# Performance work log

Measured on AMD Instinct MI355X. Metric: run time of the kernel, lower is better.

The kernel has to match this reference:

```python
import jax, jax.numpy as jnp
import numpy as np

SEQ_LEN, BATCH, INPUT, HID, LAYERS, TARGET_LEN = 120, 2048, 6, 64, 4, 120


def _cell(x_t, h, c, Wih, Whh, b):
    # torch LSTM gate order: input, forget, cell(g), output
    gates = x_t @ Wih.T + h @ Whh.T + b  # [B, 4H]
    i, f, g, o = jnp.split(gates, 4, axis=-1)
    c_new = jax.nn.sigmoid(f) * c + jax.nn.sigmoid(i) * jnp.tanh(g)
    h_new = jax.nn.sigmoid(o) * jnp.tanh(c_new)
    return h_new, c_new


def _stack_step(h, c, x_t, Wih0, Wih, Whh, b):
    # one time step through all stacked layers; h, c: [L, B, H]
    hs, cs = [], []
    inp = x_t
    L = Whh.shape[0]
    for l in range(L):
        W = Wih0 if l == 0 else Wih[l - 1]
        hn, cn = _cell(inp, h[l], c[l], W, Whh[l], b[l])
        hs.append(hn)
        cs.append(cn)
        inp = hn
    return jnp.stack(hs), jnp.stack(cs), inp


def setup_inputs() -> dict:
    key = jax.random.key(0)
    ks = jax.random.split(key, 11)
    s = 1.0 / np.sqrt(HID)  # torch LSTM uniform init scale
    u = lambda k, shp: jax.random.uniform(k, shp, jnp.float32, -s, s)
    return {
        "x": jax.random.normal(ks[0], (SEQ_LEN, BATCH, INPUT), jnp.float32),
        "enc_Wih0": u(ks[1], (4 * HID, INPUT)),
        "enc_Wih": u(ks[2], (LAYERS - 1, 4 * HID, HID)),
        "enc_Whh": u(ks[3], (LAYERS, 4 * HID, HID)),
        "enc_b": u(ks[4], (LAYERS, 4 * HID)),
        "dec_Wih0": u(ks[5], (4 * HID, INPUT)),
        "dec_Wih": u(ks[6], (LAYERS - 1, 4 * HID, HID)),
        "dec_Whh": u(ks[7], (LAYERS, 4 * HID, HID)),
        "dec_b": u(ks[8], (LAYERS, 4 * HID)),
        "lin_W": u(ks[9], (INPUT, HID)),
        "lin_b": u(ks[10], (INPUT,)),
        "target_len": TARGET_LEN,
    }


def reference(x, enc_Wih0, enc_Wih, enc_Whh, enc_b,
              dec_Wih0, dec_Wih, dec_Whh, dec_b, lin_W, lin_b, target_len):
    L, B, H = enc_Whh.shape[0], x.shape[1], enc_Whh.shape[-1]
    h0 = jnp.zeros((L, B, H), x.dtype)

    # ---- encoder: stacked LSTM over the input sequence (zero init state) ----
    def enc_step(carry, x_t):
        h, c = carry
        h, c, _ = _stack_step(h, c, x_t, enc_Wih0, enc_Wih, enc_Whh, enc_b)
        return (h, c), None

    (h, c), _ = jax.lax.scan(enc_step, (h0, h0), x)

    # ---- decoder: recursive one-step decode for target_len steps ----
    def dec_step(carry, _):
        h, c, inp = carry
        h, c, top = _stack_step(h, c, inp, dec_Wih0, dec_Wih, dec_Whh, dec_b)
        out = top @ lin_W.T + lin_b  # [B, INPUT]
        return (h, c, out), out

    last_in = x[-1]  # decoder seeded with last observed frame
    _, outputs = jax.lax.scan(dec_step, (h, c, last_in), None, length=target_len)
    return outputs  # [target_len, B, INPUT]
```

## Files before the change

### kernel.cpp

```cpp
#include <hip/hip_runtime.h>


#define S_LEN 120
#define BATCH 2048
#define NIN   6
#define H     64
#define NL    4
#define TLEN  120

#define HPAD 72

#define FRAGS_HALF 60
#define PACK_H8    (2 * FRAGS_HALF * 4 * 64)
#define PROJ_H8    (2 * 64)
#define NPACK      ((PACK_H8 + PROJ_H8) * 8)
#define EPACK_EL   (256 * 64 * 8)
#define NTOT       (NPACK + EPACK_EL)

#define WS_HOFF (768 * 1024)
#define WS_COFF (WS_HOFF + 1024 * 1024)

#define PERM(kk) ((((kk) & 3) << 4) | ((kk) >> 2))
#define PI(c)    ((((c) & 15) << 2) | ((c) >> 4))

typedef _Float16 h8    __attribute__((ext_vector_type(8)));
typedef _Float16 hh2   __attribute__((ext_vector_type(2)));
typedef float    f32x4 __attribute__((ext_vector_type(4)));

__device__ __forceinline__ void bar_lgkm() {
  asm volatile("s_waitcnt lgkmcnt(0)\n\ts_barrier" ::: "memory");
}

__global__ void prep_weights(const float* __restrict__ eWih0,
                             const float* __restrict__ eWih,
                             const float* __restrict__ eWhh,
                             const float* __restrict__ dWih0,
                             const float* __restrict__ dWih,
                             const float* __restrict__ dWhh,
                             const float* __restrict__ linW,
                             _Float16* __restrict__ wq) {
  int idx = blockIdx.x * blockDim.x + threadIdx.x;
  if (idx >= NTOT) return;

  if (idx >= NPACK) {
    int p    = idx - NPACK;
    int j    = p & 7;
    int lane = (p >> 3) & 63;
    int fe   = p >> 9;
    int kt   = fe & 3, nt = (fe >> 2) & 15, l = fe >> 6;
    int g    = nt * 16 + (lane & 15);
    int koff = ((lane >> 4) << 3) + j;
    float v = 0.0f;
    if (l == 0) {
      if (kt == 0)      v = (koff < NIN) ? eWih0[g * NIN + koff] : 0.0f;
      else if (kt == 1) v = 0.0f;
      else { int kk = (kt - 2) * 32 + koff; v = eWhh[g * H + PERM(kk)]; }
    } else {
      if (kt < 2) { int kk = kt * 32 + koff;
                    v = eWih[((l - 1) * 256 + g) * H + PERM(kk)]; }
      else        { int kk = (kt - 2) * 32 + koff;
                    v = eWhh[(l * 256 + g) * H + PERM(kk)]; }
    }
    wq[idx] = (_Float16)v;
    return;
  }

  if (idx >= PACK_H8 * 8) {
    int p    = idx - PACK_H8 * 8;
    int j    = p & 7;
    int lane = (p >> 3) & 63;
    int fr   = p >> 9;
    int m    = lane & 15;
    int k    = fr * 32 + ((lane >> 4) << 3) + j;
    wq[idx] = (_Float16)((m < NIN) ? linW[m * H + k] : 0.0f);
    return;
  }

  const int j    = idx & 7;
  const int lane = (idx >> 3) & 63;
  const int wv   = (idx >> 9) & 3;
  const int fh   = idx >> 11;
  const int f    = fh % FRAGS_HALF;
  const int half = fh / FRAGS_HALF;
  const float* Wi0 = half ? dWih0 : eWih0;
  const float* Wi  = half ? dWih  : eWih;
  const float* Wh  = half ? dWhh  : eWhh;
  int l, q, kt;
  if (f < 12) { l = 0; q = f / 3; kt = f % 3; }
  else        { int ff = f - 12; l = 1 + ff / 16; ff %= 16; q = ff / 4; kt = ff % 4; }
  const int g    = q * 64 + wv * 16 + (lane & 15);
  const int k_in = ((lane >> 4) << 3) + j;
  float v;
  if (l == 0) {
    if (kt == 0) v = (k_in < NIN) ? Wi0[g * NIN + k_in] : 0.0f;
    else         v = Wh[g * H + (kt - 1) * 32 + k_in];
  } else {
    if (kt < 2) v = Wi[((l - 1) * 256 + g) * H + kt * 32 + k_in];
    else        v = Wh[(l * 256 + g) * H + (kt - 2) * 32 + k_in];
  }
  wq[idx] = (_Float16)v;
}

__device__ __forceinline__ float rcpf(float x) { return __builtin_amdgcn_rcpf(x); }
__device__ __forceinline__ f32x4 mf(h8 a, h8 b, f32x4 c) {
  return __builtin_amdgcn_mfma_f32_16x16x32_f16(a, b, c, 0, 0, 0);
}
#define SPLAT(v) ((f32x4){(v), (v), (v), (v)})

__device__ __forceinline__ float ew_one(float gi, float gf, float gg, float go,
                                        float& c) {
  gg = fminf(fmaxf(gg, -20.0f), 20.0f);
  float eni = __expf(-gi);
  float e2g = __expf(2.0f * gg);
  float enf = __expf(-gf);
  float eno = __expf(-go);
  c = c * rcpf(1.0f + enf) + (e2g - 1.0f) * rcpf((1.0f + eni) * (e2g + 1.0f));
  float cc = fminf(fmaxf(c, -20.0f), 20.0f);
  float e2c = __expf(2.0f * cc);
  return (e2c - 1.0f) * rcpf((1.0f + eno) * (e2c + 1.0f));
}

__device__ __forceinline__ void cell_ew(f32x4 g0, f32x4 g1, f32x4 g2, f32x4 g3,
                                        f32x4& c, _Float16* outbuf,
                                        int quad, int r16, int lw) {
  #pragma unroll
  for (int r = 0; r < 4; r++) {
    float cv = c[r];
    float hv = ew_one(g0[r], g1[r], g2[r], g3[r], cv);
    c[r] = cv;
    outbuf[(quad * 4 + r) * HPAD + lw * 16 + r16] = (_Float16)hv;
  }
}
__device__ __forceinline__ void fireH(const h8 (&w)[16], h8 ai0, h8 ai1,
                                      const f32x4 (&ac)[4], f32x4& c,
                                      _Float16* outbuf, int quad, int r16, int lw) {
  f32x4 g0 = mf(ai1, w[1],  mf(ai0, w[0],  ac[0]));
  f32x4 g1 = mf(ai1, w[5],  mf(ai0, w[4],  ac[1]));
  f32x4 g2 = mf(ai1, w[9],  mf(ai0, w[8],  ac[2]));
  f32x4 g3 = mf(ai1, w[13], mf(ai0, w[12], ac[3]));
  cell_ew(g0, g1, g2, g3, c, outbuf, quad, r16, lw);
}
__device__ __forceinline__ void precH(const h8 (&w)[16], h8 ar0, h8 ar1,
                                      f32x4 b, f32x4 (&ac)[4]) {
  ac[0] = mf(ar1, w[3],  mf(ar0, w[2],  SPLAT(b[0])));
  ac[1] = mf(ar1, w[7],  mf(ar0, w[6],  SPLAT(b[1])));
  ac[2] = mf(ar1, w[11], mf(ar0, w[10], SPLAT(b[2])));
  ac[3] = mf(ar1, w[15], mf(ar0, w[14], SPLAT(b[3])));
}
__device__ __forceinline__ void fire0(const h8 (&w)[12], h8 ax,
                                      const f32x4 (&ac)[4], f32x4& c,
                                      _Float16* outbuf, int quad, int r16, int lw) {
  f32x4 g0 = mf(ax, w[0], ac[0]);
  f32x4 g1 = mf(ax, w[3], ac[1]);
  f32x4 g2 = mf(ax, w[6], ac[2]);
  f32x4 g3 = mf(ax, w[9], ac[3]);
  cell_ew(g0, g1, g2, g3, c, outbuf, quad, r16, lw);
}
__device__ __forceinline__ void prec0(const h8 (&w)[12], h8 ar0, h8 ar1,
                                      f32x4 b, f32x4 (&ac)[4]) {
  ac[0] = mf(ar1, w[2],  mf(ar0, w[1],  SPLAT(b[0])));
  ac[1] = mf(ar1, w[5],  mf(ar0, w[4],  SPLAT(b[1])));
  ac[2] = mf(ar1, w[8],  mf(ar0, w[7],  SPLAT(b[2])));
  ac[3] = mf(ar1, w[11], mf(ar0, w[10], SPLAT(b[3])));
}
__device__ __forceinline__ void readA(const _Float16* buf, int r16, int quad,
                                      h8& a0, h8& a1) {
  a0 = *(const h8*)(buf + r16 * HPAD + quad * 8);
  a1 = *(const h8*)(buf + r16 * HPAD + 32 + quad * 8);
}

__global__ void __launch_bounds__(512, 2)
lstm_enc(const float* __restrict__ X,
         const float* __restrict__ encb,
         const h8* __restrict__ WQ,
         _Float16* __restrict__ hG,
         float* __restrict__ cG) {
  __shared__ _Float16 Hb[NL][2][16][HPAD];
  __shared__ _Float16 Xb[2][16][HPAD];

  const int tid  = threadIdx.x;
  const int wv   = tid >> 6;
  const int lane = tid & 63;
  const int quad = lane >> 4;
  const int r16  = lane & 15;
  const int grp  = wv >> 2;
  const int lw   = wv & 3;
  const int bbase = blockIdx.x * 16;

  {
    float* p = (float*)&Hb[0][0][0][0];
    for (int i = tid; i < 4608; i += 512) p[i] = 0.0f;
    float* px = (float*)&Xb[0][0][0];
    for (int i = tid; i < 1152; i += 512) if (i < 1152) px[i] = 0.0f;
  }
  if (tid < 16 * NIN) {
    int m = tid / NIN, ii = tid - m * NIN;
    Xb[0][m][ii] = (_Float16)X[((size_t)0 * BATCH + bbase + m) * NIN + ii];
  }

  h8 we[8][4];
  #pragma unroll
  for (int q = 0; q < 4; q++)
    #pragma unroll
    for (int cc = 0; cc < 2; cc++)
      #pragma unroll
      for (int kt = 0; kt < 4; kt++)
        we[q * 2 + cc][kt] =
            WQ[(PACK_H8 + PROJ_H8) +
               ((lw * 64 + (q * 4 + 2 * grp + cc) * 4 + kt) * 64 + lane)];
  float ben[8];
  #pragma unroll
  for (int q = 0; q < 4; q++)
    #pragma unroll
    for (int cc = 0; cc < 2; cc++)
      ben[q * 2 + cc] = encb[lw * 256 + q * 64 + (2 * grp + cc) * 16 + r16];

  f32x4 ce[2];
  ce[0] = SPLAT(0.f); ce[1] = SPLAT(0.f);

  const bool pfLane = (wv == 0) && (lane < 48);
  const int  pe0 = lane * 2, pe1 = pe0 + 1;
  const int  pm0 = pe0 / NIN, pc0 = pe0 % NIN;
  const int  pm1 = pe1 / NIN, pc1 = pe1 % NIN;
  float pf0 = 0.f, pf1 = 0.f;
  if (pfLane) {
    const float* xs = X + ((size_t)1 * BATCH + bbase) * NIN;
    pf0 = xs[pe0]; pf1 = xs[pe1];
  }

  __syncthreads();

  #pragma unroll 1
  for (int i = 0; i < S_LEN + NL - 1; i++) {
    const int p = i & 1;
    const bool active = (i >= lw) && (i - lw < S_LEN);
    if (active) {
      const _Float16* inb = (lw == 0) ? &Xb[p][0][0] : &Hb[lw - 1][p ^ 1][0][0];
      const _Float16* rcb = &Hb[lw][p ^ 1][0][0];
      h8 ai0 = *(const h8*)(inb + r16 * HPAD + quad * 8);
      h8 ai1 = {};
      if (lw) ai1 = *(const h8*)(inb + r16 * HPAD + 32 + quad * 8);
      h8 ar0 = *(const h8*)(rcb + r16 * HPAD + quad * 8);
      h8 ar1 = *(const h8*)(rcb + r16 * HPAD + 32 + quad * 8);

      float nf0 = 0.f, nf1 = 0.f;
      if (pfLane && (i + 2 < S_LEN)) {
        const float* xs = X + ((size_t)(i + 2) * BATCH + bbase) * NIN;
        nf0 = xs[pe0]; nf1 = xs[pe1];
      }

      f32x4 a[8];
      #pragma unroll
      for (int j = 0; j < 8; j++) {
        f32x4 t = SPLAT(ben[j]);
        t = mf(ai0, we[j][0], t);
        if (lw) t = mf(ai1, we[j][1], t);
        t = mf(ar0, we[j][2], t);
        t = mf(ar1, we[j][3], t);
        a[j] = t;
      }

      _Float16* wb = &Hb[lw][p][0][0];
      #pragma unroll
      for (int r = 0; r < 4; r++) {
        hh2 hv;
        #pragma unroll
        for (int cc = 0; cc < 2; cc++) {
          float cv = ce[cc][r];
          hv[cc] = (_Float16)ew_one(a[cc][r], a[2 + cc][r],
                                    a[4 + cc][r], a[6 + cc][r], cv);
          ce[cc][r] = cv;
        }
        *(hh2*)(wb + (quad * 4 + r) * HPAD + 4 * r16 + 2 * grp) = hv;
      }

      if (pfLane && (i + 1 < S_LEN)) {
        Xb[p ^ 1][pm0][pc0] = (_Float16)pf0;
        Xb[p ^ 1][pm1][pc1] = (_Float16)pf1;
      }
      pf0 = nf0; pf1 = nf1;
    }
    bar_lgkm();
  }

  #pragma unroll
  for (int cc = 0; cc < 2; cc++)
    #pragma unroll
    for (int r = 0; r < 4; r++)
      cG[((size_t)lw * BATCH + bbase + quad * 4 + r) * H +
         (2 * grp + cc) * 16 + r16] = ce[cc][r];

  #pragma unroll
  for (int u = 0; u < 8; u++) {
    int i2 = tid + u * 512;
    int c = i2 & 63, m = (i2 >> 6) & 15, l = (i2 >> 10) & 3;
    hG[((size_t)l * BATCH + bbase + m) * H + c] =
        Hb[l][(l + 1) & 1][m][PI(c)];
  }
}

__global__ void __launch_bounds__(256, 1)
lstm_dec(const float* __restrict__ X,
         const float* __restrict__ decb,
         const float* __restrict__ linb,
         const h8* __restrict__ WQ,
         const _Float16* __restrict__ hG,
         const float* __restrict__ cG,
         float* __restrict__ out) {
  __shared__ _Float16 Hb[NL][2][16][HPAD];

  const int tid   = threadIdx.x;
  const int lw    = tid >> 6;
  const int lane  = tid & 63;
  const int quad  = lane >> 4;
  const int r16   = lane & 15;
  const int bbase = blockIdx.x * 16;

  #pragma unroll
  for (int u = 0; u < 16; u++) {
    int i2 = tid + u * 256;
    int l = i2 >> 10, m = (i2 >> 6) & 15, c = i2 & 63;
    Hb[l][1][m][c] = hG[((size_t)l * BATCH + bbase + m) * H + c];
  }

  f32x4 cs0, cs1, cs2, cs3;
  #pragma unroll
  for (int r = 0; r < 4; r++) {
    cs0[r] = cG[((size_t)0 * BATCH + bbase + quad * 4 + r) * H + lw * 16 + r16];
    cs1[r] = cG[((size_t)1 * BATCH + bbase + quad * 4 + r) * H + lw * 16 + r16];
    cs2[r] = cG[((size_t)2 * BATCH + bbase + quad * 4 + r) * H + lw * 16 + r16];
    cs3[r] = cG[((size_t)3 * BATCH + bbase + quad * 4 + r) * H + lw * 16 + r16];
  }

  h8 w0[12], w1[16], w2[16], w3[16];
  #pragma unroll
  for (int f = 0; f < 12; f++) w0[f] = WQ[((FRAGS_HALF + f)      * 4 + lw) * 64 + lane];
  #pragma unroll
  for (int f = 0; f < 16; f++) w1[f] = WQ[((FRAGS_HALF + 12 + f) * 4 + lw) * 64 + lane];
  #pragma unroll
  for (int f = 0; f < 16; f++) w2[f] = WQ[((FRAGS_HALF + 28 + f) * 4 + lw) * 64 + lane];
  #pragma unroll
  for (int f = 0; f < 16; f++) w3[f] = WQ[((FRAGS_HALF + 44 + f) * 4 + lw) * 64 + lane];

  f32x4 b0, b1, b2, b3;
  #pragma unroll
  for (int q = 0; q < 4; q++) {
    b0[q] = decb[0 * 256 + q * 64 + lw * 16 + r16];
    b1[q] = decb[1 * 256 + q * 64 + lw * 16 + r16];
    b2[q] = decb[2 * 256 + q * 64 + lw * 16 + r16];
    b3[q] = decb[3 * 256 + q * 64 + lw * 16 + r16];
  }

  h8 lwA0 = WQ[PACK_H8 + lane];
  h8 lwA1 = WQ[PACK_H8 + 64 + lane];
  f32x4 lbq;
  #pragma unroll
  for (int r = 0; r < 4; r++)
    lbq[r] = (quad * 4 + r < NIN) ? linb[quad * 4 + r] : 0.0f;

  h8 xseed = {};
  if (quad == 0) {
    const float* xs = X + ((size_t)(S_LEN - 1) * BATCH + bbase + r16) * NIN;
    #pragma unroll
    for (int j = 0; j < 6; j++) xseed[j] = (_Float16)xs[j];
  }

  __syncthreads();

  f32x4 ac0[4], ac1[4], ac2[4], ac3[4];
  {
    h8 s0, s1;
    readA(&Hb[0][1][0][0], r16, quad, s0, s1); prec0(w0, s0, s1, b0, ac0);
    readA(&Hb[1][1][0][0], r16, quad, s0, s1); precH(w1, s0, s1, b1, ac1);
    readA(&Hb[2][1][0][0], r16, quad, s0, s1); precH(w2, s0, s1, b2, ac2);
  }

  #pragma unroll 1
  for (int t = 0; t < TLEN; t++) {
    const int cur = t & 1, prv = cur ^ 1;
    {
      h8 ar0, ar1;
      readA(&Hb[3][prv][0][0], r16, quad, ar0, ar1);
      h8 ax;
      if (t == 0) {
        ax = xseed;
      } else {
        f32x4 ap = lbq;
        ap = mf(lwA0, ar0, ap);
        ap = mf(lwA1, ar1, ap);
        if (lw == 0) {
          #pragma unroll
          for (int r = 0; r < 4; r++) {
            const int fm = quad * 4 + r;
            if (fm < NIN)
              out[((size_t)(t - 1) * BATCH + bbase + r16) * NIN + fm] = ap[r];
          }
        }
        float x0 = __shfl(ap[0], r16);
        float x1 = __shfl(ap[1], r16);
        float x2 = __shfl(ap[2], r16);
        float x3 = __shfl(ap[3], r16);
        float x4 = __shfl(ap[0], 16 + r16);
        float x5 = __shfl(ap[1], 16 + r16);
        h8 xa = {};
        xa[0] = (_Float16)x0; xa[1] = (_Float16)x1; xa[2] = (_Float16)x2;
        xa[3] = (_Float16)x3; xa[4] = (_Float16)x4; xa[5] = (_Float16)x5;
        h8 zz = {};
        ax = (quad == 0) ? xa : zz;
      }
      precH(w3, ar0, ar1, b3, ac3);
      fire0(w0, ax, ac0, cs0, &Hb[0][cur][0][0], quad, r16, lw);
      bar_lgkm();
    }
    {
      h8 ai0, ai1;
      readA(&Hb[0][cur][0][0], r16, quad, ai0, ai1);
      fireH(w1, ai0, ai1, ac1, cs1, &Hb[1][cur][0][0], quad, r16, lw);
      prec0(w0, ai0, ai1, b0, ac0);
      bar_lgkm();
    }
    {
      h8 ai0, ai1;
      readA(&Hb[1][cur][0][0], r16, quad, ai0, ai1);
      fireH(w2, ai0, ai1, ac2, cs2, &Hb[2][cur][0][0], quad, r16, lw);
      precH(w1, ai0, ai1, b1, ac1);
      bar_lgkm();
    }
    {
      h8 ai0, ai1;
      readA(&Hb[2][cur][0][0], r16, quad, ai0, ai1);
      fireH(w3, ai0, ai1, ac3, cs3, &Hb[3][cur][0][0], quad, r16, lw);
      precH(w2, ai0, ai1, b2, ac2);
      bar_lgkm();
    }
  }

  if (lw == 0) {
    h8 ar0, ar1;
    readA(&Hb[3][1][0][0], r16, quad, ar0, ar1);
    f32x4 ap = lbq;
    ap = mf(lwA0, ar0, ap);
    ap = mf(lwA1, ar1, ap);
    #pragma unroll
    for (int r = 0; r < 4; r++) {
      const int fm = quad * 4 + r;
      if (fm < NIN)
        out[((size_t)(TLEN - 1) * BATCH + bbase + r16) * NIN + fm] = ap[r];
    }
  }
}

extern "C" void kernel_launch(void* const* d_in, const int* in_sizes, int n_in,
                              void* d_out, int out_size, void* d_ws, size_t ws_size,
                              hipStream_t stream) {
  const float* X     = (const float*)d_in[0];
  const float* eWih0 = (const float*)d_in[1];
  const float* eWih  = (const float*)d_in[2];
  const float* eWhh  = (const float*)d_in[3];
  const float* eb    = (const float*)d_in[4];
  const float* dWih0 = (const float*)d_in[5];
  const float* dWih  = (const float*)d_in[6];
  const float* dWhh  = (const float*)d_in[7];
  const float* db    = (const float*)d_in[8];
  const float* lW    = (const float*)d_in[9];
  const float* lb    = (const float*)d_in[10];

  _Float16* wq = (_Float16*)d_ws;
  _Float16* hG = (_Float16*)((char*)d_ws + WS_HOFF);
  float*    cG = (float*)((char*)d_ws + WS_COFF);

  prep_weights<<<(NTOT + 255) / 256, 256, 0, stream>>>(
      eWih0, eWih, eWhh, dWih0, dWih, dWhh, lW, wq);

  lstm_enc<<<BATCH / 16, 512, 0, stream>>>(
      X, eb, (const h8*)wq, hG, cG);

  lstm_dec<<<BATCH / 16, 256, 0, stream>>>(
      X, db, lb, (const h8*)wq, hG, cG, (float*)d_out);
}
```

Baseline: 566.0 us.

## Shrink per-block batch tile to raise block count in encoder and decoder

The encoder now handles 8 batch rows per block instead of 16, and the decoder 4 rows instead of 16. Block counts rise to 256 and 512, so more CUs are busy on this latency-bound recurrence. In the encoder, lanes split the MFMA output rows with a cross-half shuffle so each lane runs fewer elementwise gate updates. The decoder still runs full 16-row MFMA tiles filled with replicated rows, so it repeats work to gain parallelism, and the extra shuffles add per-step latency.

```diff
diff --git a/kernel.cpp b/kernel.cpp
--- a/kernel.cpp
+++ b/kernel.cpp
@@ -185,15 +185,17 @@
   const int r16  = lane & 15;
   const int grp  = wv >> 2;
   const int lw   = wv & 3;
-  const int bbase = blockIdx.x * 16;
+  const bool hi  = quad >= 2;
+  const int rowA = hi ? (quad - 2) * 4 + 2 : quad * 4;
+  const int bbase = blockIdx.x * 8;
 
   {
     float* p = (float*)&Hb[0][0][0][0];
     for (int i = tid; i < 4608; i += 512) p[i] = 0.0f;
     float* px = (float*)&Xb[0][0][0];
-    for (int i = tid; i < 1152; i += 512) if (i < 1152) px[i] = 0.0f;
-  }
-  if (tid < 16 * NIN) {
+    for (int i = tid; i < 1152; i += 512) px[i] = 0.0f;
+  }
+  if (tid < 8 * NIN) {
     int m = tid / NIN, ii = tid - m * NIN;
     Xb[0][m][ii] = (_Float16)X[((size_t)0 * BATCH + bbase + m) * NIN + ii];
   }
@@ -215,18 +217,14 @@
     for (int cc = 0; cc < 2; cc++)
       ben[q * 2 + cc] = encb[lw * 256 + q * 64 + (2 * grp + cc) * 16 + r16];
 
-  f32x4 ce[2];
-  ce[0] = SPLAT(0.f); ce[1] = SPLAT(0.f);
+  float2 ce2[2];
+  ce2[0] = make_float2(0.f, 0.f);
+  ce2[1] = make_float2(0.f, 0.f);
 
   const bool pfLane = (wv == 0) && (lane < 48);
-  const int  pe0 = lane * 2, pe1 = pe0 + 1;
-  const int  pm0 = pe0 / NIN, pc0 = pe0 % NIN;
-  const int  pm1 = pe1 / NIN, pc1 = pe1 % NIN;
-  float pf0 = 0.f, pf1 = 0.f;
-  if (pfLane) {
-    const float* xs = X + ((size_t)1 * BATCH + bbase) * NIN;
-    pf0 = xs[pe0]; pf1 = xs[pe1];
-  }
+  const int  pm = lane / NIN, pc = lane - pm * NIN;
+  float pf = 0.f;
+  if (pfLane) pf = X[((size_t)1 * BATCH + bbase + pm) * NIN + pc];
 
   __syncthreads();
 
@@ -243,11 +241,9 @@
       h8 ar0 = *(const h8*)(rcb + r16 * HPAD + quad * 8);
       h8 ar1 = *(const h8*)(rcb + r16 * HPAD + 32 + quad * 8);
 
-      float nf0 = 0.f, nf1 = 0.f;
-      if (pfLane && (i + 2 < S_LEN)) {
-        const float* xs = X + ((size_t)(i + 2) * BATCH + bbase) * NIN;
-        nf0 = xs[pe0]; nf1 = xs[pe1];
-      }
+      float nf = 0.f;
+      if (pfLane && (i + 2 < S_LEN))
+        nf = X[((size_t)(i + 2) * BATCH + bbase + pm) * NIN + pc];
 
       f32x4 a[8];
       #pragma unroll
@@ -260,25 +256,31 @@
         a[j] = t;
       }
 
+      float va[8][2];
+      #pragma unroll
+      for (int j = 0; j < 8; j++) {
+        float t2 = __shfl_xor(a[j][2], 32);
+        float t3 = __shfl_xor(a[j][3], 32);
+        va[j][0] = hi ? t2 : a[j][0];
+        va[j][1] = hi ? t3 : a[j][1];
+      }
+
       _Float16* wb = &Hb[lw][p][0][0];
       #pragma unroll
-      for (int r = 0; r < 4; r++) {
+      for (int s = 0; s < 2; s++) {
         hh2 hv;
         #pragma unroll
         for (int cc = 0; cc < 2; cc++) {
-          float cv = ce[cc][r];
-          hv[cc] = (_Float16)ew_one(a[cc][r], a[2 + cc][r],
-                                    a[4 + cc][r], a[6 + cc][r], cv);
-          ce[cc][r] = cv;
+          float cv = s ? ce2[cc].y : ce2[cc].x;
+          hv[cc] = (_Float16)ew_one(va[cc][s], va[2 + cc][s],
+                                    va[4 + cc][s], va[6 + cc][s], cv);
+          if (s) ce2[cc].y = cv; else ce2[cc].x = cv;
         }
-        *(hh2*)(wb + (quad * 4 + r) * HPAD + 4 * r16 + 2 * grp) = hv;
+        *(hh2*)(wb + (rowA + s) * HPAD + 4 * r16 + 2 * grp) = hv;
       }
 
-      if (pfLane && (i + 1 < S_LEN)) {
-        Xb[p ^ 1][pm0][pc0] = (_Float16)pf0;
-        Xb[p ^ 1][pm1][pc1] = (_Float16)pf1;
-      }
-      pf0 = nf0; pf1 = nf1;
+      if (pfLane && (i + 1 < S_LEN)) Xb[p ^ 1][pm][pc] = (_Float16)pf;
+      pf = nf;
     }
     bar_lgkm();
   }
@@ -286,14 +288,14 @@
   #pragma unroll
   for (int cc = 0; cc < 2; cc++)
     #pragma unroll
-    for (int r = 0; r < 4; r++)
-      cG[((size_t)lw * BATCH + bbase + quad * 4 + r) * H +
-         (2 * grp + cc) * 16 + r16] = ce[cc][r];
-
-  #pragma unroll
-  for (int u = 0; u < 8; u++) {
+    for (int s = 0; s < 2; s++)
+      cG[((size_t)lw * BATCH + bbase + rowA + s) * H +
+         (2 * grp + cc) * 16 + r16] = s ? ce2[cc].y : ce2[cc].x;
+
+  #pragma unroll
+  for (int u = 0; u < 4; u++) {
     int i2 = tid + u * 512;
-    int c = i2 & 63, m = (i2 >> 6) & 15, l = (i2 >> 10) & 3;
+    int c = i2 & 63, m = (i2 >> 6) & 7, l = i2 >> 9;
     hG[((size_t)l * BATCH + bbase + m) * H + c] =
         Hb[l][(l + 1) & 1][m][PI(c)];
   }
@@ -314,22 +316,23 @@
   const int lane  = tid & 63;
   const int quad  = lane >> 4;
   const int r16   = lane & 15;
-  const int bbase = blockIdx.x * 16;
+  const int bbase = blockIdx.x * 4;
 
   #pragma unroll
   for (int u = 0; u < 16; u++) {
     int i2 = tid + u * 256;
     int l = i2 >> 10, m = (i2 >> 6) & 15, c = i2 & 63;
-    Hb[l][1][m][c] = hG[((size_t)l * BATCH + bbase + m) * H + c];
+    Hb[l][1][m][c] = hG[((size_t)l * BATCH + bbase + (m & 3)) * H + c];
   }
 
   f32x4 cs0, cs1, cs2, cs3;
   #pragma unroll
   for (int r = 0; r < 4; r++) {
-    cs0[r] = cG[((size_t)0 * BATCH + bbase + quad * 4 + r) * H + lw * 16 + r16];
-    cs1[r] = cG[((size_t)1 * BATCH + bbase + quad * 4 + r) * H + lw * 16 + r16];
-    cs2[r] = cG[((size_t)2 * BATCH + bbase + quad * 4 + r) * H + lw * 16 + r16];
-    cs3[r] = cG[((size_t)3 * BATCH + bbase + quad * 4 + r) * H + lw * 16 + r16];
+    const int m = (quad * 4 + r) & 3;
+    cs0[r] = cG[((size_t)0 * BATCH + bbase + m) * H + lw * 16 + r16];
+    cs1[r] = cG[((size_t)1 * BATCH + bbase + m) * H + lw * 16 + r16];
+    cs2[r] = cG[((size_t)2 * BATCH + bbase + m) * H + lw * 16 + r16];
+    cs3[r] = cG[((size_t)3 * BATCH + bbase + m) * H + lw * 16 + r16];
   }
 
   h8 w0[12], w1[16], w2[16], w3[16];
@@ -359,7 +362,7 @@
     lbq[r] = (quad * 4 + r < NIN) ? linb[quad * 4 + r] : 0.0f;
 
   h8 xseed = {};
-  if (quad == 0) {
+  if (quad == 0 && r16 < 4) {
     const float* xs = X + ((size_t)(S_LEN - 1) * BATCH + bbase + r16) * NIN;
     #pragma unroll
     for (int j = 0; j < 6; j++) xseed[j] = (_Float16)xs[j];
@@ -388,7 +391,7 @@
         f32x4 ap = lbq;
         ap = mf(lwA0, ar0, ap);
         ap = mf(lwA1, ar1, ap);
-        if (lw == 0) {
+        if (lw == 0 && r16 < 4) {
           #pragma unroll
           for (int r = 0; r < 4; r++) {
             const int fm = quad * 4 + r;
@@ -441,11 +444,13 @@
     f32x4 ap = lbq;
     ap = mf(lwA0, ar0, ap);
     ap = mf(lwA1, ar1, ap);
-    #pragma unroll
-    for (int r = 0; r < 4; r++) {
-      const int fm = quad * 4 + r;
-      if (fm < NIN)
-        out[((size_t)(TLEN - 1) * BATCH + bbase + r16) * NIN + fm] = ap[r];
+    if (r16 < 4) {
+      #pragma unroll
+      for (int r = 0; r < 4; r++) {
+        const int fm = quad * 4 + r;
+        if (fm < NIN)
+          out[((size_t)(TLEN - 1) * BATCH + bbase + r16) * NIN + fm] = ap[r];
+      }
     }
   }
 }
@@ -472,9 +477,9 @@
   prep_weights<<<(NTOT + 255) / 256, 256, 0, stream>>>(
       eWih0, eWih, eWhh, dWih0, dWih, dWhh, lW, wq);
 
-  lstm_enc<<<BATCH / 16, 512, 0, stream>>>(
+  lstm_enc<<<BATCH / 8, 512, 0, stream>>>(
       X, eb, (const h8*)wq, hG, cG);
 
-  lstm_dec<<<BATCH / 16, 256, 0, stream>>>(
+  lstm_dec<<<BATCH / 4, 256, 0, stream>>>(
       X, db, lb, (const h8*)wq, hG, cG, (float*)d_out);
 }
```

New measurement: 793.5 us. +40.2%, slower.
